# Optimization experiments

Measured on AMD Instinct MI355X. Metric: run time of the kernel, lower is better.

## Reference

```python
import jax, jax.numpy as jnp
import numpy as np

NUM_HEADS = 12

def setup_inputs() -> dict:
    key = jax.random.key(0)
    ks = jax.random.split(key, 6)
    B, N, C = 8, 1024, 768
    x = jax.random.normal(ks[0], (B, N, C), dtype=jnp.float32)
    qkv_w = jax.random.normal(ks[1], (3 * C, C), dtype=jnp.float32) * 0.02
    qkv_b = jax.random.normal(ks[2], (3 * C,), dtype=jnp.float32) * 0.02
    static_a = jax.random.normal(ks[3], (1, NUM_HEADS, N, N), dtype=jnp.float32) * 0.02
    proj_w = jax.random.normal(ks[4], (C, C), dtype=jnp.float32) * 0.02
    proj_b = jax.random.normal(ks[5], (C,), dtype=jnp.float32) * 0.02
    return {"x": x, "qkv_w": qkv_w, "qkv_b": qkv_b, "static_a": static_a,
            "proj_w": proj_w, "proj_b": proj_b}

def reference(x, qkv_w, qkv_b, static_a, proj_w, proj_b):
    B, N, C = x.shape
    H = NUM_HEADS
    D = C // H
    scale = D ** -0.5
    # qkv: [B,N,3C] -> [3,B,H,N,D]
    qkv = (x @ qkv_w.T + qkv_b).reshape(B, N, 3, H, D).transpose(2, 0, 3, 1, 4)
    q, k, v = qkv[0], qkv[1], qkv[2]
    attn = jnp.einsum('bhnd,bhmd->bhnm', q, k) * scale
    attn = jax.nn.softmax(attn, axis=-1)
    attn = attn + static_a  # static bias added AFTER softmax (no renorm)
    out = jnp.einsum('bhnm,bhmd->bhnd', attn, v)  # [B,H,N,D]
    out = out.transpose(0, 2, 1, 3).reshape(B, N, C)
    return out @ proj_w.T + proj_b
```

## Files before the change

### kernel.cpp

```cpp
#include <hip/hip_runtime.h>
#include <math.h>

#define NB   8
#define SEQ  1024
#define CH   768
#define NH   12
#define HD   64
#define BHT  (NB * NH)
#define QKVN 2304

typedef unsigned short u16;
typedef unsigned int   u32;
typedef __attribute__((ext_vector_type(8))) short bf16x8;
typedef __attribute__((ext_vector_type(4))) float f32x4;

__device__ __forceinline__ float bf2f(u32 s) {
    union { u32 u; float f; } v; v.u = s << 16; return v.f;
}
__device__ __forceinline__ u16 f2bf(float f) {
    union { float f; u32 u; } v; v.f = f;
    u32 u = v.u;
    return (u16)((u + 0x7fffu + ((u >> 16) & 1u)) >> 16);
}
__device__ __forceinline__ u32 cvtpk(float lo, float hi) {
    u32 r;
    asm("v_cvt_pk_bf16_f32 %0, %1, %2" : "=v"(r) : "v"(lo), "v"(hi));
    return r;
}
__device__ __forceinline__ float ld1(const u16* p) { return bf2f((u32)*p); }
__device__ __forceinline__ void st1(u16* p, float v) { *p = f2bf(v); }
__device__ __forceinline__ void st4v(u16* p, float a, float b, float c, float d) {
    ushort4 o; o.x = f2bf(a); o.y = f2bf(b); o.z = f2bf(c); o.w = f2bf(d);
    *(ushort4*)p = o;
}
__device__ __forceinline__ void st4v(float* p, float a, float b, float c, float d) {
    float4 o; o.x = a; o.y = b; o.z = c; o.w = d;
    *(float4*)p = o;
}
__device__ __forceinline__ void gload16(const u16* g, u16* l) {
    __builtin_amdgcn_global_load_lds(
        (const __attribute__((address_space(1))) void*)g,
        (__attribute__((address_space(3))) void*)l, 16, 0, 0);
}

__global__ void detect_kernel(const u32* __restrict__ x, int* __restrict__ flag) {
    __shared__ int cnt;
    if (threadIdx.x == 0) cnt = 0;
    __syncthreads();
    int c = 0;
    for (int i = threadIdx.x; i < 2048; i += 256) {
        const u32 e0 = (x[i] >> 7) & 0xFFu;
        c += (e0 >= 110u && e0 <= 132u) ? 1 : 0;
    }
    atomicAdd(&cnt, c);
    __syncthreads();
    if (threadIdx.x == 0) *flag = (cnt > 1024) ? 1 : 0;
}

#define PREP_V4 5309184
__device__ __forceinline__ void prep_seg(size_t v, const size_t e0[6],
                                         int* segp, size_t* offp) {
    int seg = 5;
    if      (v < 1572864) seg = 0;
    else if (v < 2015232) seg = 1;
    else if (v < 2015808) seg = 2;
    else if (v < 5161536) seg = 3;
    else if (v < 5308992) seg = 4;
    *segp = seg; *offp = v * 4 - e0[seg];
}

__global__ __launch_bounds__(256) void prep_all(
    const int* __restrict__ flag,
    const void* __restrict__ s0, const void* __restrict__ s1, const void* __restrict__ s2,
    const void* __restrict__ s3, const void* __restrict__ s4, const void* __restrict__ s5,
    u16* __restrict__ dst)
{
    const size_t e0[6] = {0, 6291456, 8060928, 8063232, 20646144, 21235968};
    if (*flag != 0) {
        const u16* const srcs[6] = {(const u16*)s0, (const u16*)s1, (const u16*)s2,
                                    (const u16*)s3, (const u16*)s4, (const u16*)s5};
        for (size_t v = blockIdx.x * 256 + threadIdx.x; v < PREP_V4; v += (size_t)gridDim.x * 256) {
            int seg; size_t off;
            prep_seg(v, e0, &seg, &off);
            *(ushort4*)(dst + v * 4) = *(const ushort4*)(srcs[seg] + off);
        }
    } else {
        const float* const srcs[6] = {(const float*)s0, (const float*)s1, (const float*)s2,
                                      (const float*)s3, (const float*)s4, (const float*)s5};
        for (size_t v = blockIdx.x * 256 + threadIdx.x; v < PREP_V4; v += (size_t)gridDim.x * 256) {
            int seg; size_t off;
            prep_seg(v, e0, &seg, &off);
            const float4 f = *(const float4*)(srcs[seg] + off);
            ushort4 o; o.x = f2bf(f.x); o.y = f2bf(f.y); o.z = f2bf(f.z); o.w = f2bf(f.w);
            *(ushort4*)(dst + v * 4) = o;
        }
    }
}

template<bool SWAP>
__device__ __forceinline__ void gemm128_core(
    const u16* __restrict__ Ag, const u16* __restrict__ Bg,
    f32x4 acc[4][4], u16* As, u16* Bs, int wm, int wn, int l15, int quad)
{
    const int t = threadIdx.x;
    const int w = t >> 6, lane = t & 63;
    const int lr = lane >> 2, lc = lane & 3;
    const int r0 = w * 16 + lr;
    const int r1 = 64 + w * 16 + lr;
    const int g0 = (lc + r0) & 3, g1 = (lc + r1) & 3;
    const u16* a0 = Ag + (size_t)r0 * CH + g0 * 8;
    const u16* a1 = Ag + (size_t)r1 * CH + g1 * 8;
    const u16* b0 = Bg + (size_t)r0 * CH + g0 * 8;
    const u16* b1 = Bg + (size_t)r1 * CH + g1 * 8;
    u16* lA0 = As + w * 512;
    u16* lA1 = As + 2048 + w * 512;
    u16* lB0 = Bs + w * 512;
    u16* lB1 = Bs + 2048 + w * 512;

#pragma unroll
    for (int mi = 0; mi < 4; mi++)
#pragma unroll
        for (int ni = 0; ni < 4; ni++) { f32x4 z = {0.f,0.f,0.f,0.f}; acc[mi][ni] = z; }

    for (int k0 = 0; k0 < CH; k0 += 32) {
        __syncthreads();
        gload16(a0 + k0, lA0);
        gload16(a1 + k0, lA1);
        gload16(b0 + k0, lB0);
        gload16(b1 + k0, lB1);
        __syncthreads();
        bf16x8 af[4], bfr[4];
#pragma unroll
        for (int mi = 0; mi < 4; mi++) {
            const int ra = wm * 64 + mi * 16 + l15;
            af[mi] = *(const bf16x8*)&As[ra * 32 + ((quad - ra) & 3) * 8];
        }
#pragma unroll
        for (int ni = 0; ni < 4; ni++) {
            const int rb = wn * 64 + ni * 16 + l15;
            bfr[ni] = *(const bf16x8*)&Bs[rb * 32 + ((quad - rb) & 3) * 8];
        }
#pragma unroll
        for (int mi = 0; mi < 4; mi++)
#pragma unroll
            for (int ni = 0; ni < 4; ni++)
                acc[mi][ni] = SWAP
                    ? __builtin_amdgcn_mfma_f32_16x16x32_bf16(bfr[ni], af[mi], acc[mi][ni], 0, 0, 0)
                    : __builtin_amdgcn_mfma_f32_16x16x32_bf16(af[mi], bfr[ni], acc[mi][ni], 0, 0, 0);
    }
}

__global__ __launch_bounds__(256) void qkv_gemm(
    const u16* __restrict__ x, const u16* __restrict__ w, const u16* __restrict__ bias,
    u16* __restrict__ Qn, u16* __restrict__ Kn, u16* __restrict__ Vt)
{
    __shared__ u16 As[128 * 32];
    __shared__ u16 Bs[128 * 32];
    const int t = threadIdx.x, lane = t & 63, wv = t >> 6;
    const int l15 = lane & 15, quad = lane >> 4;
    const int wm = wv >> 1, wn = wv & 1;
    const int m0 = blockIdx.y * 128, n0 = blockIdx.x * 128;
    const int which = n0 / CH;
    const int h     = ((n0 % CH) >> 6) + wn;
    const int b     = m0 >> 10;
    const size_t bh = (size_t)b * NH + h;
    const int sq0   = m0 & 1023;
    f32x4 acc[4][4];

    if (which == 2) {
        gemm128_core<false>(x + (size_t)m0 * CH, w + (size_t)n0 * CH,
                            acc, As, Bs, wm, wn, l15, quad);
        float bv[4];
#pragma unroll
        for (int ni = 0; ni < 4; ni++) bv[ni] = ld1(bias + n0 + wn * 64 + ni * 16 + l15);
#pragma unroll
        for (int mi = 0; mi < 4; mi++) {
            const int seq = sq0 + wm * 64 + mi * 16 + quad * 4;
#pragma unroll
            for (int ni = 0; ni < 4; ni++) {
                const int d = ni * 16 + l15;
                st4v(&Vt[(bh * HD + d) * SEQ + seq],
                     acc[mi][ni][0] + bv[ni], acc[mi][ni][1] + bv[ni],
                     acc[mi][ni][2] + bv[ni], acc[mi][ni][3] + bv[ni]);
            }
        }
    } else {
        gemm128_core<true>(x + (size_t)m0 * CH, w + (size_t)n0 * CH,
                           acc, As, Bs, wm, wn, l15, quad);
        u16* T2 = which ? Kn : Qn;
        const float qsc = which ? 1.0f : 0.18033688011112042f;
        float bvr[4][4];
#pragma unroll
        for (int ni = 0; ni < 4; ni++)
#pragma unroll
            for (int r = 0; r < 4; r++)
                bvr[ni][r] = ld1(bias + n0 + wn * 64 + ni * 16 + quad * 4 + r);
#pragma unroll
        for (int mi = 0; mi < 4; mi++) {
            const int seq = sq0 + wm * 64 + mi * 16 + l15;
#pragma unroll
            for (int ni = 0; ni < 4; ni++) {
                const int dbase = ni * 16 + quad * 4;
                st4v(&T2[(bh * SEQ + seq) * HD + dbase],
                     (acc[mi][ni][0] + bvr[ni][0]) * qsc,
                     (acc[mi][ni][1] + bvr[ni][1]) * qsc,
                     (acc[mi][ni][2] + bvr[ni][2]) * qsc,
                     (acc[mi][ni][3] + bvr[ni][3]) * qsc);
            }
        }
    }
}

__global__ __launch_bounds__(256) void attn_kernel(
    const u16* __restrict__ Qn, const u16* __restrict__ Kn, const u16* __restrict__ Vt,
    const u16* __restrict__ Ab, u16* __restrict__ AO)
{
    __shared__ u16 Ks[64 * 72];
    __shared__ u16 Vs[64 * 72];
    __shared__ u16 Ps[4 * 32 * 72];

    const int qb = blockIdx.x;
    const int y  = blockIdx.y;
    const int hh = y >> 3, b = y & 7;
    const size_t bh = (size_t)b * NH + hh;
    const int t  = threadIdx.x;
    const int w  = t >> 6, lane = t & 63;
    const int l15 = lane & 15, quad = lane >> 4;
    const int sr = t >> 2, sc = (t & 3) * 16;
    const int i0g = qb * 128 + w * 32;
    u16* Psw = Ps + w * 32 * 72;

    bf16x8 qa[2][2];
#pragma unroll
    for (int isub = 0; isub < 2; isub++)
#pragma unroll
        for (int db = 0; db < 2; db++)
            qa[isub][db] = *(const bf16x8*)(Qn +
                (bh * SEQ + i0g + isub * 16 + l15) * HD + db * 32 + quad * 8);

    f32x4 Op[2][4], Oa[2][4];
#pragma unroll
    for (int i = 0; i < 2; i++)
#pragma unroll
        for (int d = 0; d < 4; d++) { f32x4 z = {0.f,0.f,0.f,0.f}; Op[i][d] = z; Oa[i][d] = z; }
    float rl[2][4] = {{0.f,0.f,0.f,0.f},{0.f,0.f,0.f,0.f}};

    for (int kt = 0; kt < 16; kt++) {
        const int j0 = kt * 64;
        bf16x8 afr[2][2];
#pragma unroll
        for (int jb = 0; jb < 2; jb++)
#pragma unroll
            for (int isub = 0; isub < 2; isub++)
                afr[jb][isub] = *(const bf16x8*)(Ab +
                    ((size_t)hh * SEQ + i0g + isub * 16 + l15) * SEQ
                    + j0 + jb * 32 + quad * 8);

        const u16* kp = Kn + (bh * SEQ + j0 + sr) * HD + sc;
        const u16* vp = Vt + (bh * HD + sr) * SEQ + j0 + sc;
        const uint4 k0v = *(const uint4*)kp, k1v = *(const uint4*)(kp + 8);
        const uint4 v0v = *(const uint4*)vp, v1v = *(const uint4*)(vp + 8);
        __syncthreads();
        *(uint4*)&Ks[sr * 72 + sc] = k0v; *(uint4*)&Ks[sr * 72 + sc + 8] = k1v;
        *(uint4*)&Vs[sr * 72 + sc] = v0v; *(uint4*)&Vs[sr * 72 + sc + 8] = v1v;
        __syncthreads();

#pragma unroll
        for (int j16 = 0; j16 < 4; j16++) {
            const bf16x8 kf0 = *(const bf16x8*)&Ks[(j16 * 16 + l15) * 72 + quad * 8];
            const bf16x8 kf1 = *(const bf16x8*)&Ks[(j16 * 16 + l15) * 72 + 32 + quad * 8];
#pragma unroll
            for (int isub = 0; isub < 2; isub++) {
                f32x4 s = {0.f, 0.f, 0.f, 0.f};
                s = __builtin_amdgcn_mfma_f32_16x16x32_bf16(qa[isub][0], kf0, s, 0, 0, 0);
                s = __builtin_amdgcn_mfma_f32_16x16x32_bf16(qa[isub][1], kf1, s, 0, 0, 0);
#pragma unroll
                for (int r = 0; r < 4; r++) {
                    const float p = exp2f(fminf(s[r], 86.6f));
                    rl[isub][r] += p;
                    Psw[(isub * 16 + quad * 4 + r) * 72 + j16 * 16 + l15] = (u16)cvtpk(p, p);
                }
            }
        }

#pragma unroll
        for (int jb = 0; jb < 2; jb++) {
            bf16x8 pf[2];
#pragma unroll
            for (int isub = 0; isub < 2; isub++)
                pf[isub] = *(const bf16x8*)&Psw[(isub * 16 + l15) * 72 + jb * 32 + quad * 8];
#pragma unroll
            for (int d16 = 0; d16 < 4; d16++) {
                const bf16x8 vf = *(const bf16x8*)&Vs[(d16 * 16 + l15) * 72 + jb * 32 + quad * 8];
#pragma unroll
                for (int isub = 0; isub < 2; isub++) {
                    Op[isub][d16] = __builtin_amdgcn_mfma_f32_16x16x32_bf16(vf, pf[isub], Op[isub][d16], 0, 0, 0);
                    Oa[isub][d16] = __builtin_amdgcn_mfma_f32_16x16x32_bf16(vf, afr[jb][isub], Oa[isub][d16], 0, 0, 0);
                }
            }
        }
    }

    float inv[2];
#pragma unroll
    for (int isub = 0; isub < 2; isub++) {
        float rr[4];
#pragma unroll
        for (int r = 0; r < 4; r++) {
            float v = rl[isub][r];
            v += __shfl_xor(v, 1); v += __shfl_xor(v, 2);
            v += __shfl_xor(v, 4); v += __shfl_xor(v, 8);
            rr[r] = v;
        }
        const int src = (l15 >> 2) << 4;
        const float t0 = __shfl(rr[0], src), t1 = __shfl(rr[1], src);
        const float t2 = __shfl(rr[2], src), t3 = __shfl(rr[3], src);
        const float sel = (l15 & 2) ? ((l15 & 1) ? t3 : t2)
                                    : ((l15 & 1) ? t1 : t0);
        inv[isub] = 1.f / sel;
    }
#pragma unroll
    for (int isub = 0; isub < 2; isub++) {
        const int n = i0g + isub * 16 + l15;
#pragma unroll
        for (int d16 = 0; d16 < 4; d16++)
            st4v(&AO[((size_t)b * SEQ + n) * CH + hh * HD + d16 * 16 + quad * 4],
                 Op[isub][d16][0] * inv[isub] + Oa[isub][d16][0],
                 Op[isub][d16][1] * inv[isub] + Oa[isub][d16][1],
                 Op[isub][d16][2] * inv[isub] + Oa[isub][d16][2],
                 Op[isub][d16][3] * inv[isub] + Oa[isub][d16][3]);
    }
}

__global__ __launch_bounds__(256) void proj_all(
    const int* __restrict__ flag,
    const u16* __restrict__ AO, const u16* __restrict__ w, const u16* __restrict__ bias,
    void* __restrict__ outv)
{
    __shared__ u16 As[128 * 32];
    __shared__ u16 Bs[128 * 32];
    const int isbf = *flag;
    const int t = threadIdx.x, lane = t & 63, wv = t >> 6;
    const int l15 = lane & 15, quad = lane >> 4;
    const int wm = wv >> 1, wn = wv & 1;
    const int m0 = blockIdx.y * 128, n0 = blockIdx.x * 128;

    f32x4 acc[4][4];
    gemm128_core<true>(AO + (size_t)m0 * CH, w + (size_t)n0 * CH,
                       acc, As, Bs, wm, wn, l15, quad);

    float bvr[4][4];
#pragma unroll
    for (int ni = 0; ni < 4; ni++)
#pragma unroll
        for (int r = 0; r < 4; r++)
            bvr[ni][r] = ld1(bias + n0 + wn * 64 + ni * 16 + quad * 4 + r);
#pragma unroll
    for (int mi = 0; mi < 4; mi++) {
        const int m = m0 + wm * 64 + mi * 16 + l15;
#pragma unroll
        for (int ni = 0; ni < 4; ni++) {
            const int n = n0 + wn * 64 + ni * 16 + quad * 4;
            if (isbf)
                st4v((u16*)outv + (size_t)m * CH + n,
                     acc[mi][ni][0] + bvr[ni][0], acc[mi][ni][1] + bvr[ni][1],
                     acc[mi][ni][2] + bvr[ni][2], acc[mi][ni][3] + bvr[ni][3]);
            else
                st4v((float*)outv + (size_t)m * CH + n,
                     acc[mi][ni][0] + bvr[ni][0], acc[mi][ni][1] + bvr[ni][1],
                     acc[mi][ni][2] + bvr[ni][2], acc[mi][ni][3] + bvr[ni][3]);
        }
    }
}

extern "C" void kernel_launch(void* const* d_in, const int* in_sizes, int n_in,
                              void* d_out, int out_size, void* d_ws, size_t ws_size,
                              hipStream_t stream) {
    (void)in_sizes; (void)n_in; (void)out_size; (void)ws_size;
    u16* ws = (u16*)d_ws;
    u16* xb   = ws;
    u16* wqb  = ws + 6291456;
    u16* bqb  = ws + 8060928;
    u16* Ab   = ws + 8063232;
    u16* pwb  = ws + 20646144;
    u16* pbb  = ws + 21235968;
    u16* arena_end = ws + 21236736;
    const size_t S1 = (size_t)NB * NH * SEQ * HD;
    u16* Qn = arena_end;
    u16* Kn = Qn + S1;
    u16* Vt = Kn + S1;
    u16* AO = Vt + S1;
    int* flag = (int*)(AO + S1);

    detect_kernel<<<dim3(1), dim3(256), 0, stream>>>((const u32*)d_in[0], flag);

    const dim3 blk(256);
    prep_all<<<dim3(4096), blk, 0, stream>>>(flag,
        d_in[0], d_in[1], d_in[2], d_in[3], d_in[4], d_in[5], ws);

    qkv_gemm<<<dim3(QKVN / 128, (NB * SEQ) / 128), blk, 0, stream>>>(
        xb, wqb, bqb, Qn, Kn, Vt);
    attn_kernel<<<dim3(SEQ / 128, BHT), blk, 0, stream>>>(Qn, Kn, Vt, Ab, AO);

    proj_all<<<dim3(CH / 128, (NB * SEQ) / 128), blk, 0, stream>>>(
        flag, AO, pwb, pbb, d_out);
}
```

Measured before the change: 280.7 us.

## Shrink proj tile to 128x64, remap blocks per XCD, switch softmax exp to natural base

The projection GEMM moves to a new 128x64 tile core, which doubles its grid so the MI355X compute units are better filled. Both the QKV and projection GEMMs remap block indices so that neighbouring M tiles land on the same XCD, aiming for better L2 reuse of the A rows. The attention softmax now uses __expf with a plain 1/8 Q scale instead of exp2f with a log2e-folded scale, and it packs bf16 with a software rounding routine instead of the v_cvt_pk instruction. The smaller tile lowers per-block reuse of the weights, and the software bf16 conversion may cost more ALU work in the inner loop.

```diff
diff --git a/kernel.cpp b/kernel.cpp
--- a/kernel.cpp
+++ b/kernel.cpp
@@ -22,13 +22,7 @@
     u32 u = v.u;
     return (u16)((u + 0x7fffu + ((u >> 16) & 1u)) >> 16);
 }
-__device__ __forceinline__ u32 cvtpk(float lo, float hi) {
-    u32 r;
-    asm("v_cvt_pk_bf16_f32 %0, %1, %2" : "=v"(r) : "v"(lo), "v"(hi));
-    return r;
-}
 __device__ __forceinline__ float ld1(const u16* p) { return bf2f((u32)*p); }
-__device__ __forceinline__ void st1(u16* p, float v) { *p = f2bf(v); }
 __device__ __forceinline__ void st4v(u16* p, float a, float b, float c, float d) {
     ushort4 o; o.x = f2bf(a); o.y = f2bf(b); o.z = f2bf(c); o.w = f2bf(d);
     *(ushort4*)p = o;
@@ -150,16 +144,70 @@
     }
 }
 
+template<bool SWAP>
+__device__ __forceinline__ void gemm128x64_core(
+    const u16* __restrict__ Ag, const u16* __restrict__ Bg,
+    f32x4 acc[4][2], u16* As, u16* Bs, int wm, int wn, int l15, int quad)
+{
+    const int t = threadIdx.x;
+    const int w = t >> 6, lane = t & 63;
+    const int lr = lane >> 2, lc = lane & 3;
+    const int r0 = w * 16 + lr;
+    const int r1 = 64 + w * 16 + lr;
+    const int g0 = (lc + r0) & 3, g1 = (lc + r1) & 3;
+    const u16* a0 = Ag + (size_t)r0 * CH + g0 * 8;
+    const u16* a1 = Ag + (size_t)r1 * CH + g1 * 8;
+    const u16* b0 = Bg + (size_t)r0 * CH + g0 * 8;
+    u16* lA0 = As + w * 512;
+    u16* lA1 = As + 2048 + w * 512;
+    u16* lB0 = Bs + w * 512;
+
+#pragma unroll
+    for (int mi = 0; mi < 4; mi++)
+#pragma unroll
+        for (int ni = 0; ni < 2; ni++) { f32x4 z = {0.f,0.f,0.f,0.f}; acc[mi][ni] = z; }
+
+    for (int k0 = 0; k0 < CH; k0 += 32) {
+        __syncthreads();
+        gload16(a0 + k0, lA0);
+        gload16(a1 + k0, lA1);
+        gload16(b0 + k0, lB0);
+        __syncthreads();
+        bf16x8 af[4], bfr[2];
+#pragma unroll
+        for (int mi = 0; mi < 4; mi++) {
+            const int ra = wm * 64 + mi * 16 + l15;
+            af[mi] = *(const bf16x8*)&As[ra * 32 + ((quad - ra) & 3) * 8];
+        }
+#pragma unroll
+        for (int ni = 0; ni < 2; ni++) {
+            const int rb = wn * 32 + ni * 16 + l15;
+            bfr[ni] = *(const bf16x8*)&Bs[rb * 32 + ((quad - rb) & 3) * 8];
+        }
+#pragma unroll
+        for (int mi = 0; mi < 4; mi++)
+#pragma unroll
+            for (int ni = 0; ni < 2; ni++)
+                acc[mi][ni] = SWAP
+                    ? __builtin_amdgcn_mfma_f32_16x16x32_bf16(bfr[ni], af[mi], acc[mi][ni], 0, 0, 0)
+                    : __builtin_amdgcn_mfma_f32_16x16x32_bf16(af[mi], bfr[ni], acc[mi][ni], 0, 0, 0);
+    }
+}
+
 __global__ __launch_bounds__(256) void qkv_gemm(
     const u16* __restrict__ x, const u16* __restrict__ w, const u16* __restrict__ bias,
     u16* __restrict__ Qn, u16* __restrict__ Kn, u16* __restrict__ Vt)
 {
     __shared__ u16 As[128 * 32];
     __shared__ u16 Bs[128 * 32];
+    const int id  = blockIdx.y * 18 + blockIdx.x;
+    const int xcd = id & 7, seq0 = id >> 3;
+    const int by  = xcd * 8 + seq0 / 18;
+    const int bx  = seq0 % 18;
     const int t = threadIdx.x, lane = t & 63, wv = t >> 6;
     const int l15 = lane & 15, quad = lane >> 4;
     const int wm = wv >> 1, wn = wv & 1;
-    const int m0 = blockIdx.y * 128, n0 = blockIdx.x * 128;
+    const int m0 = by * 128, n0 = bx * 128;
     const int which = n0 / CH;
     const int h     = ((n0 % CH) >> 6) + wn;
     const int b     = m0 >> 10;
@@ -188,7 +236,7 @@
         gemm128_core<true>(x + (size_t)m0 * CH, w + (size_t)n0 * CH,
                            acc, As, Bs, wm, wn, l15, quad);
         u16* T2 = which ? Kn : Qn;
-        const float qsc = which ? 1.0f : 0.18033688011112042f;
+        const float qsc = which ? 1.0f : 0.125f;
         float bvr[4][4];
 #pragma unroll
         for (int ni = 0; ni < 4; ni++)
@@ -276,9 +324,9 @@
                 s = __builtin_amdgcn_mfma_f32_16x16x32_bf16(qa[isub][1], kf1, s, 0, 0, 0);
 #pragma unroll
                 for (int r = 0; r < 4; r++) {
-                    const float p = exp2f(fminf(s[r], 86.6f));
+                    const float p = __expf(fminf(s[r], 60.f));
                     rl[isub][r] += p;
-                    Psw[(isub * 16 + quad * 4 + r) * 72 + j16 * 16 + l15] = (u16)cvtpk(p, p);
+                    Psw[(isub * 16 + quad * 4 + r) * 72 + j16 * 16 + l15] = f2bf(p);
                 }
             }
         }
@@ -338,29 +386,33 @@
     void* __restrict__ outv)
 {
     __shared__ u16 As[128 * 32];
-    __shared__ u16 Bs[128 * 32];
+    __shared__ u16 Bs[64 * 32];
     const int isbf = *flag;
+    const int id  = blockIdx.y * 12 + blockIdx.x;
+    const int xcd = id & 7, seq0 = id >> 3;
+    const int by  = xcd * 8 + seq0 / 12;
+    const int bx  = seq0 % 12;
     const int t = threadIdx.x, lane = t & 63, wv = t >> 6;
     const int l15 = lane & 15, quad = lane >> 4;
     const int wm = wv >> 1, wn = wv & 1;
-    const int m0 = blockIdx.y * 128, n0 = blockIdx.x * 128;
-
-    f32x4 acc[4][4];
-    gemm128_core<true>(AO + (size_t)m0 * CH, w + (size_t)n0 * CH,
-                       acc, As, Bs, wm, wn, l15, quad);
-
-    float bvr[4][4];
-#pragma unroll
-    for (int ni = 0; ni < 4; ni++)
+    const int m0 = by * 128, n0 = bx * 64;
+
+    f32x4 acc[4][2];
+    gemm128x64_core<true>(AO + (size_t)m0 * CH, w + (size_t)n0 * CH,
+                          acc, As, Bs, wm, wn, l15, quad);
+
+    float bvr[2][4];
+#pragma unroll
+    for (int ni = 0; ni < 2; ni++)
 #pragma unroll
         for (int r = 0; r < 4; r++)
-            bvr[ni][r] = ld1(bias + n0 + wn * 64 + ni * 16 + quad * 4 + r);
+            bvr[ni][r] = ld1(bias + n0 + wn * 32 + ni * 16 + quad * 4 + r);
 #pragma unroll
     for (int mi = 0; mi < 4; mi++) {
         const int m = m0 + wm * 64 + mi * 16 + l15;
 #pragma unroll
-        for (int ni = 0; ni < 4; ni++) {
-            const int n = n0 + wn * 64 + ni * 16 + quad * 4;
+        for (int ni = 0; ni < 2; ni++) {
+            const int n = n0 + wn * 32 + ni * 16 + quad * 4;
             if (isbf)
                 st4v((u16*)outv + (size_t)m * CH + n,
                      acc[mi][ni][0] + bvr[ni][0], acc[mi][ni][1] + bvr[ni][1],
@@ -402,6 +454,6 @@
         xb, wqb, bqb, Qn, Kn, Vt);
     attn_kernel<<<dim3(SEQ / 128, BHT), blk, 0, stream>>>(Qn, Kn, Vt, Ab, AO);
 
-    proj_all<<<dim3(CH / 128, (NB * SEQ) / 128), blk, 0, stream>>>(
+    proj_all<<<dim3(CH / 64, (NB * SEQ) / 128), blk, 0, stream>>>(
         flag, AO, pwb, pbb, d_out);
 }
```

Result: faster. 271.0 us, median of 3 (-3.5%).
